# Kernel optimization log

Hardware: AMD Instinct MI355X
Metric: run time of the kernel (lower is better)

## Reference

```python
import jax, jax.numpy as jnp
import numpy as np

EPS = 1e-5
SLOPE = 0.2


def _conv(x, w, b, stride, pad):
    y = jax.lax.conv_general_dilated(
        x, w, (stride, stride), ((pad, pad), (pad, pad)),
        dimension_numbers=('NCHW', 'OIHW', 'NCHW'))
    return y + b[None, :, None, None]


def _inorm(x):
    m = x.mean(axis=(2, 3), keepdims=True)
    v = x.var(axis=(2, 3), keepdims=True)
    return (x - m) * jax.lax.rsqrt(v + EPS)


def _down(x, w, b, norm):
    y = _conv(x, w, b, 2, 1)
    if norm:
        y = _inorm(y)
    return jax.nn.leaky_relu(y, SLOPE)


def _self_attn(x, wq, bq, wk, bk, wv, bv, gamma):
    B, C, H, W = x.shape
    N = H * W
    q = _conv(x, wq, bq, 1, 0).reshape(B, -1, N)   # (B, C/8, N)
    k = _conv(x, wk, bk, 1, 0).reshape(B, -1, N)
    v = _conv(x, wv, bv, 1, 0).reshape(B, C, N)
    attn = jax.nn.softmax(jnp.einsum('bcn,bcm->bnm', q, k), axis=-1)  # (B,N,N)
    out = jnp.einsum('bcm,bnm->bcn', v, attn).reshape(B, C, H, W)
    return gamma * out + x


def _branch(p, img):
    (w0, b0, w1, b1, w2, b2, wq, bq, wk, bk, wv, bv, gamma, wh, bh) = p
    x = _down(img, w0, b0, norm=False)
    x = _down(x, w1, b1, norm=True)
    x = _self_attn(x, wq, bq, wk, bk, wv, bv, gamma)
    x = _down(x, w2, b2, norm=True)
    return _conv(x, wh, bh, 1, 1)  # head: Conv2d(nf*4, 1, 4, padding=1)


def setup_inputs() -> dict:
    key = jax.random.key(0)
    ks = jax.random.split(key, 20)
    S, B, H = 4, 16, 128
    s = 0.05  # weight scale for numerical stability of softmax energies
    d = {
        'img': jax.random.normal(ks[0], (B, 1, H, H), jnp.float32),
        'stage_idx': jax.random.randint(ks[1], (B,), 0, S, jnp.int32),
        'w0': jax.random.normal(ks[2], (S, 64, 1, 4, 4)) * s,
        'b0': jax.random.normal(ks[3], (S, 64)) * s,
        'w1': jax.random.normal(ks[4], (S, 128, 64, 4, 4)) * s,
        'b1': jax.random.normal(ks[5], (S, 128)) * s,
        'w2': jax.random.normal(ks[6], (S, 256, 128, 4, 4)) * s,
        'b2': jax.random.normal(ks[7], (S, 256)) * s,
        'wq': jax.random.normal(ks[8], (S, 16, 128, 1, 1)) * s,
        'bq': jax.random.normal(ks[9], (S, 16)) * s,
        'wk': jax.random.normal(ks[10], (S, 16, 128, 1, 1)) * s,
        'bk': jax.random.normal(ks[11], (S, 16)) * s,
        'wv': jax.random.normal(ks[12], (S, 128, 128, 1, 1)) * s,
        'bv': jax.random.normal(ks[13], (S, 128)) * s,
        'gamma': jax.random.normal(ks[14], (S,)) * s,
        'wh': jax.random.normal(ks[15], (S, 1, 256, 4, 4)) * s,
        'bh': jax.random.normal(ks[16], (S, 1)) * s,
    }
    return d


def reference(img, stage_idx, w0, b0, w1, b1, w2, b2, wq, bq, wk, bk, wv, bv, gamma, wh, bh):
    params = (w0, b0, w1, b1, w2, b2, wq, bq, wk, bk, wv, bv, gamma, wh, bh)
    # compute every branch for every sample (as the original), stacked over stage axis
    all_preds = jax.vmap(_branch, in_axes=(0, None))(params, img)  # (S, B, 1, h, w)
    B = img.shape[0]
    return all_preds[stage_idx, jnp.arange(B)]  # (B, 1, h, w)
```

## Files before the change

kernel.cpp:

```cpp
#include <hip/hip_runtime.h>

#define LRELU(x) ((x) > 0.0f ? (x) : 0.2f * (x))
#define SB __builtin_amdgcn_sched_barrier(0)

typedef short bf16x8 __attribute__((ext_vector_type(8)));
typedef short bf16x4 __attribute__((ext_vector_type(4)));
typedef float f32x4 __attribute__((ext_vector_type(4)));

__device__ __forceinline__ short f2bf(float f) {
  union { float f; unsigned u; } x{f};
  return (short)((x.u + 0x7FFF + ((x.u >> 16) & 1)) >> 16);
}

__global__ __launch_bounds__(256) void k_repack_all(
    const float* __restrict__ w1, unsigned short* __restrict__ wr1,
    const float* __restrict__ w2, unsigned short* __restrict__ wr2,
    const float* __restrict__ bh, const int* __restrict__ sidx,
    float* __restrict__ out, unsigned short* __restrict__ x0t,
    unsigned short* __restrict__ ybf, const float* __restrict__ img,
    const float* __restrict__ w0, const float* __restrict__ b0) {
  __shared__ float Ish[4 * 34];
  if (blockIdx.x >= 2837) {
    const int t = threadIdx.x;
    const int q = blockIdx.x - 2837;
    const int b = q >> 8, py = q & 255;
    const int oh = py >> 2, owb = (py & 3) << 4;
    const int s = sidx[b];
    const float* ip = img + (size_t)b * 16384;
    if (t < 136) {
      int r = t / 34, c = t % 34;
      int ih = 2 * oh - 1 + r, iw = 2 * owb - 1 + c;
      Ish[t] = ((unsigned)ih < 128u && (unsigned)iw < 128u) ? ip[ih * 128 + iw] : 0.f;
    }
    const int co = t & 63, ps = t >> 6;
    float wreg[16];
    const float* wp = w0 + (s * 64 + co) * 16;
#pragma unroll
    for (int i = 0; i < 16; i++) wreg[i] = wp[i];
    float bb = b0[s * 64 + co];
    __syncthreads();
    unsigned short* op = x0t + ((size_t)b * 4356 + (oh + 1) * 66 + (owb + 1)) * 64 + co;
#pragma unroll
    for (int j = 0; j < 4; j++) {
      int pl = ps * 4 + j;
      float acc = bb;
#pragma unroll
      for (int kh = 0; kh < 4; kh++)
#pragma unroll
        for (int kw = 0; kw < 4; kw++)
          acc += wreg[kh * 4 + kw] * Ish[kh * 34 + pl * 2 + kw];
      acc = LRELU(acc);
      op[pl * 64] = (unsigned short)f2bf(acc);
    }
    return;
  }
  int idx = blockIdx.x * 256 + threadIdx.x;
  if (idx < 131072) {
    float4 v = *(const float4*)(w1 + (size_t)idx * 4);
    int base = idx * 4;
    int tap0 = base & 15;
    int rest = base >> 4;
    int ci = rest & 63, sco = rest >> 6;
    unsigned short* d = wr1 + (size_t)sco * 1024 + ci;
    d[(tap0 + 0) * 64] = (unsigned short)f2bf(v.x);
    d[(tap0 + 1) * 64] = (unsigned short)f2bf(v.y);
    d[(tap0 + 2) * 64] = (unsigned short)f2bf(v.z);
    d[(tap0 + 3) * 64] = (unsigned short)f2bf(v.w);
    return;
  } else if (idx < 655360) {
    int i = idx - 131072;
    float4 v = *(const float4*)(w2 + (size_t)i * 4);
    int base = i * 4;
    int tap0 = base & 15;
    int rest = base >> 4;
    int ci = rest & 127, sco = rest >> 7;
    unsigned short* d = wr2 + (size_t)sco * 2048 + ci;
    d[(tap0 + 0) * 128] = (unsigned short)f2bf(v.x);
    d[(tap0 + 1) * 128] = (unsigned short)f2bf(v.y);
    d[(tap0 + 2) * 128] = (unsigned short)f2bf(v.z);
    d[(tap0 + 3) * 128] = (unsigned short)f2bf(v.w);
    return;
  } else if (idx < 658960) {
    int i = idx - 655360;
    if (i < 3600) out[i] = bh[sidx[i / 225]];
    return;
  } else if (idx < 692240) {
    int i = idx - 658960;
    int b = i / 2080, r = i % 2080;
    int pix = r >> 3, sub = r & 7;
    int row, col;
    if (pix < 66) { row = 0; col = pix; }
    else if (pix < 132) { row = 65; col = pix - 66; }
    else { int qq = pix - 132; row = 1 + (qq >> 1); col = (qq & 1) * 65; }
    bf16x8 z = {0, 0, 0, 0, 0, 0, 0, 0};
    *(bf16x8*)(x0t + ((size_t)b * 4356 + row * 66 + col) * 64 + sub * 8) = z;
    return;
  } else {
    int i = idx - 692240;
    if (i >= 33792) return;
    int b = i / 2112, r = i % 2112;
    int pix = r >> 4, sub = r & 15;
    int row, col;
    if (pix < 34) { row = 0; col = pix; }
    else if (pix < 68) { row = 33; col = pix - 34; }
    else { int qq = pix - 68; row = 1 + (qq >> 1); col = (qq & 1) * 33; }
    bf16x8 z = {0, 0, 0, 0, 0, 0, 0, 0};
    *(bf16x8*)(ybf + ((size_t)b * 1156 + row * 34 + col) * 128 + sub * 8) = z;
    return;
  }
}

__global__ __launch_bounds__(256, 2) void k_conv1n(
    const unsigned short* __restrict__ x0t, const unsigned short* __restrict__ wr,
    const int* __restrict__ sidx, float* __restrict__ x1) {
  __shared__ __align__(16) unsigned short Xs[26624];
  const int t = threadIdx.x;
  const int b = blockIdx.x;
  const int y = blockIdx.y;
  const int ne = y & 15;
  const int cog = y >> 4;
  const int s = sidx[b];
  const int lane = t & 63, wv = t >> 6;
  const int quad = lane >> 4, l16 = lane & 15;

  const unsigned short* gb = x0t + ((size_t)b * 4356 + 4 * ne * 66) * 64;
  {
    float4 v[13];
#pragma unroll
    for (int i = 0; i < 13; i++) v[i] = *(const float4*)(gb + (i * 256 + t) * 8);
#pragma unroll
    for (int i = 0; i < 13; i++) {
      int ba = (i * 256 + t) * 16;
      int sw = ba ^ (((ba >> 9) & 7) << 4);
      *(float4*)((char*)Xs + sw) = v[i];
    }
  }
  __syncthreads();

  const int co0w = cog * 64 + wv * 16;
  const unsigned short* ap = wr + ((size_t)(s * 128 + co0w + l16)) * 1024 + quad * 8;
  f32x4 acc[4];
#pragma unroll
  for (int nt = 0; nt < 4; nt++) acc[nt] = (f32x4){0.f, 0.f, 0.f, 0.f};

#pragma unroll
  for (int kc = 0; kc < 32; kc++) {
    const int tap = kc >> 1;
    const int cio = (kc & 1) * 32 + quad * 8;
    const int kh = tap >> 2, kw = tap & 3;
    bf16x8 af = *(const bf16x8*)(ap + kc * 32);
#pragma unroll
    for (int nt = 0; nt < 4; nt++) {
      int lr = 2 * (nt >> 1) + kh;
      int col = 2 * ((nt & 1) * 16 + l16) + kw;
      int ba = ((lr * 66 + col) * 64 + cio) * 2;
      int sw = ba ^ (((ba >> 9) & 7) << 4);
      bf16x8 bv = *(const bf16x8*)((const char*)Xs + sw);
      acc[nt] = __builtin_amdgcn_mfma_f32_16x16x32_bf16(af, bv, acc[nt], 0, 0, 0);
    }
  }

#pragma unroll
  for (int nt = 0; nt < 4; nt++) {
    int p = ne * 64 + (nt >> 1) * 32 + (nt & 1) * 16 + l16;
#pragma unroll
    for (int r = 0; r < 4; r++)
      x1[((size_t)b * 128 + co0w + quad * 4 + r) * 1024 + p] = acc[nt][r];
  }
}

template <int NPIX>
__global__ __launch_bounds__(256) void k_inorm(float* __restrict__ x) {
  constexpr int E = NPIX / 256;
  float* p = x + (size_t)blockIdx.x * NPIX;
  const int t = threadIdx.x;
  float v[E];
  float sum = 0.f, sq = 0.f;
#pragma unroll
  for (int i = 0; i < E; i++) {
    v[i] = p[i * 256 + t];
    sum += v[i];
    sq += v[i] * v[i];
  }
#pragma unroll
  for (int o = 32; o > 0; o >>= 1) {
    sum += __shfl_down(sum, o, 64);
    sq += __shfl_down(sq, o, 64);
  }
  __shared__ float red[8];
  int wid = t >> 6;
  if ((t & 63) == 0) {
    red[wid] = sum;
    red[4 + wid] = sq;
  }
  __syncthreads();
  float S = red[0] + red[1] + red[2] + red[3];
  float SQ = red[4] + red[5] + red[6] + red[7];
  float m = S * (1.0f / NPIX);
  float var = SQ * (1.0f / NPIX) - m * m;
  float inv = rsqrtf(var + 1e-5f);
#pragma unroll
  for (int i = 0; i < E; i++) p[i * 256 + t] = LRELU((v[i] - m) * inv);
}

__global__ __launch_bounds__(256) void k_proj_qkv(
    const float* __restrict__ xin, const float* __restrict__ wq,
    const float* __restrict__ bq, const float* __restrict__ wk,
    const float* __restrict__ bk, const float* __restrict__ wv,
    const float* __restrict__ bv, const int* __restrict__ sidx,
    float* __restrict__ q, float* __restrict__ kout, unsigned short* __restrict__ vpk) {
  __shared__ float xsh[32 * 256];
  __shared__ float wsh[16 * 32];
  const int t = threadIdx.x;
  const int b = blockIdx.x;
  const int y = blockIdx.y;
  const int s = sidx[b];
  const int cg = t >> 6, ng = t & 63;
  const float* w;
  const float* bias;
  int co0, nn0, CO;
  if (y < 8) {
    w = (y < 4) ? wq : wk;
    bias = (y < 4) ? bq : bk;
    co0 = 0;
    nn0 = (y & 3) * 256;
    CO = 16;
  } else {
    w = wv;
    bias = bv;
    co0 = ((y - 8) >> 2) * 16;
    nn0 = ((y - 8) & 3) * 256;
    CO = 128;
  }
  const float* xb = xin + (size_t)b * 128 * 1024;
  float4 acc4[4];
#pragma unroll
  for (int c = 0; c < 4; c++) {
    float bb = bias[s * CO + co0 + cg * 4 + c];
    acc4[c] = make_float4(bb, bb, bb, bb);
  }
  for (int cc = 0; cc < 4; cc++) {
#pragma unroll
    for (int k = 0; k < 8; k++) {
      int id = t + (k << 8);
      int ci = id >> 6, nf = id & 63;
      ((float4*)xsh)[id] = ((const float4*)(xb + (cc * 32 + ci) * 1024 + nn0))[nf];
    }
    if (t < 128)
      ((float4*)wsh)[t] =
          ((const float4*)(w + ((size_t)(s * CO + co0 + (t >> 3))) * 128 + cc * 32))[t & 7];
    __syncthreads();
#pragma unroll
    for (int ci4 = 0; ci4 < 8; ci4++) {
      float4 wvv[4], xv[4];
#pragma unroll
      for (int c = 0; c < 4; c++) wvv[c] = ((const float4*)wsh)[(cg * 4 + c) * 8 + ci4];
#pragma unroll
      for (int i = 0; i < 4; i++) xv[i] = ((const float4*)xsh)[(ci4 * 4 + i) * 64 + ng];
#pragma unroll
      for (int c = 0; c < 4; c++)
#pragma unroll
        for (int i = 0; i < 4; i++) {
          float wvc = i == 0 ? wvv[c].x : i == 1 ? wvv[c].y : i == 2 ? wvv[c].z : wvv[c].w;
          acc4[c].x += wvc * xv[i].x;
          acc4[c].y += wvc * xv[i].y;
          acc4[c].z += wvc * xv[i].z;
          acc4[c].w += wvc * xv[i].w;
        }
    }
    __syncthreads();
  }
  if (y < 8) {
    float* out = (y < 4) ? q : kout;
#pragma unroll
    for (int c = 0; c < 4; c++)
      ((float4*)(out + ((size_t)b * 16 + cg * 4 + c) * 1024 + nn0))[ng] = acc4[c];
  } else {
    int n = nn0 + ng * 4;
#pragma unroll
    for (int c = 0; c < 4; c++) {
      int co = co0 + cg * 4 + c;
      bf16x4 u;
      u[0] = f2bf(acc4[c].x);
      u[1] = f2bf(acc4[c].y);
      u[2] = f2bf(acc4[c].z);
      u[3] = f2bf(acc4[c].w);
      *(bf16x4*)(vpk + (((size_t)b * 32 + (n >> 5)) * 128 + co) * 32 + (n & 31)) = u;
    }
  }
}

__global__ __launch_bounds__(256, 2) void k_attn(
    const float* __restrict__ q, const float* __restrict__ k,
    const unsigned short* __restrict__ vpk, const float* __restrict__ x1,
    const float* __restrict__ gamma, const int* __restrict__ sidx,
    unsigned short* __restrict__ ybf) {
  __shared__ __align__(16) short Psh[16 * 1032];
  __shared__ float qsh[256];
  __shared__ float redm[64], reds[64];
  const int t = threadIdx.x;
  const int b = blockIdx.x >> 6;
  const int n0 = (blockIdx.x & 63) << 4;
  const int lane = t & 63, wv = t >> 6;
  const int quad = lane >> 4, l16 = lane & 15;
  const float* qb = q + (size_t)b * 16 * 1024;
  const float* kb = k + (size_t)b * 16 * 1024;
  const float* xb = x1 + (size_t)b * 128 * 1024;

  qsh[t] = qb[((t >> 4) << 10) + n0 + (t & 15)];
  __syncthreads();

  float acc[4][16];
#pragma unroll
  for (int j = 0; j < 4; j++)
#pragma unroll
    for (int nl = 0; nl < 16; nl++) acc[j][nl] = 0.0f;

  float4 KA[4], KB[4];
#define LDK(BUF, G)                                                       \
  _Pragma("unroll") for (int c4 = 0; c4 < 4; c4++)                        \
      BUF[c4] = *(const float4*)(kb + ((((G) * 4 + c4)) << 10) + 4 * t);  \
  SB;
#define MMK(BUF, G)                                                                         \
  _Pragma("unroll") for (int c4 = 0; c4 < 4; c4++) {                                        \
    const float* qr = qsh + ((G) * 4 + c4) * 16;                                            \
    _Pragma("unroll") for (int j = 0; j < 4; j++) {                                         \
      float kk = j == 0 ? BUF[c4].x : j == 1 ? BUF[c4].y : j == 2 ? BUF[c4].z : BUF[c4].w;  \
      _Pragma("unroll") for (int nl = 0; nl < 16; nl++) acc[j][nl] += kk * qr[nl];          \
    }                                                                                       \
  }                                                                                         \
  SB;

  LDK(KA, 0)
  LDK(KB, 1)
  MMK(KA, 0) LDK(KA, 2)
  MMK(KB, 1) LDK(KB, 3)
  MMK(KA, 2)
  MMK(KB, 3)
#undef LDK
#undef MMK

  float lmax[16];
#pragma unroll
  for (int nl = 0; nl < 16; nl++)
    lmax[nl] = fmaxf(fmaxf(acc[0][nl], acc[1][nl]), fmaxf(acc[2][nl], acc[3][nl]));
#pragma unroll
  for (int o = 32; o > 0; o >>= 1)
#pragma unroll
    for (int nl = 0; nl < 16; nl++) lmax[nl] = fmaxf(lmax[nl], __shfl_xor(lmax[nl], o, 64));
  if (lane == 0)
#pragma unroll
    for (int nl = 0; nl < 16; nl++) redm[wv * 16 + nl] = lmax[nl];
  __syncthreads();
#pragma unroll
  for (int nl = 0; nl < 16; nl++)
    lmax[nl] = fmaxf(fmaxf(redm[nl], redm[16 + nl]), fmaxf(redm[32 + nl], redm[48 + nl]));
  float lsum[16];
#pragma unroll
  for (int nl = 0; nl < 16; nl++) lsum[nl] = 0.0f;
#pragma unroll
  for (int j = 0; j < 4; j++)
#pragma unroll
    for (int nl = 0; nl < 16; nl++) {
      float e = __expf(acc[j][nl] - lmax[nl]);
      acc[j][nl] = e;
      lsum[nl] += e;
    }
#pragma unroll
  for (int o = 32; o > 0; o >>= 1)
#pragma unroll
    for (int nl = 0; nl < 16; nl++) lsum[nl] += __shfl_xor(lsum[nl], o, 64);
  if (lane == 0)
#pragma unroll
    for (int nl = 0; nl < 16; nl++) reds[wv * 16 + nl] = lsum[nl];
#pragma unroll
  for (int nl = 0; nl < 16; nl++) {
    bf16x4 pv;
    pv[0] = f2bf(acc[0][nl]);
    pv[1] = f2bf(acc[1][nl]);
    pv[2] = f2bf(acc[2][nl]);
    pv[3] = f2bf(acc[3][nl]);
    *(bf16x4*)&Psh[nl * 1032 + 4 * t] = pv;
  }
  __syncthreads();

  const unsigned short* vp =
      vpk + ((size_t)b * 32 * 128 + (size_t)(wv * 32 + l16)) * 32 + quad * 8;
  const short* prow = Psh + l16 * 1032 + quad * 8;
  f32x4 dacc[2];
  dacc[0] = (f32x4){0.f, 0.f, 0.f, 0.f};
  dacc[1] = (f32x4){0.f, 0.f, 0.f, 0.f};

  bf16x8 VA0[4], VA1[4], PAr[4];
  bf16x8 VB0[4], VB1[4], PBr[4];
#define LDV(V0, V1, PR, G)                                \
  _Pragma("unroll") for (int m4 = 0; m4 < 4; m4++) {      \
    int mt = (G) * 4 + m4;                                \
    V0[m4] = *(const bf16x8*)(vp + mt * 4096);            \
    V1[m4] = *(const bf16x8*)(vp + 512 + mt * 4096);      \
    PR[m4] = *(const bf16x8*)(prow + mt * 32);            \
  }                                                       \
  SB;
#define MMV(V0, V1, PR)                                                                      \
  _Pragma("unroll") for (int m4 = 0; m4 < 4; m4++) {                                         \
    dacc[0] = __builtin_amdgcn_mfma_f32_16x16x32_bf16(V0[m4], PR[m4], dacc[0], 0, 0, 0);     \
    dacc[1] = __builtin_amdgcn_mfma_f32_16x16x32_bf16(V1[m4], PR[m4], dacc[1], 0, 0, 0);     \
  }                                                                                          \
  SB;

  LDV(VA0, VA1, PAr, 0)
  LDV(VB0, VB1, PBr, 1)
  MMV(VA0, VA1, PAr) LDV(VA0, VA1, PAr, 2)
  MMV(VB0, VB1, PBr) LDV(VB0, VB1, PBr, 3)
  MMV(VA0, VA1, PAr) LDV(VA0, VA1, PAr, 4)
  MMV(VB0, VB1, PBr) LDV(VB0, VB1, PBr, 5)
  MMV(VA0, VA1, PAr) LDV(VA0, VA1, PAr, 6)
  MMV(VB0, VB1, PBr) LDV(VB0, VB1, PBr, 7)
  MMV(VA0, VA1, PAr)
  MMV(VB0, VB1, PBr)
#undef LDV
#undef MMV
  __syncthreads();

  float* Osh = (float*)Psh;
  short* Osh2 = Psh + 4352;
#pragma unroll
  for (int i = 0; i < 2; i++) {
    int cob = wv * 32 + i * 16 + quad * 4;
#pragma unroll
    for (int r = 0; r < 4; r++) Osh[(cob + r) * 17 + l16] = dacc[i][r];
  }
  __syncthreads();
  float g = gamma[sidx[b]];
  {
    int co = t >> 1, j0 = (t & 1) * 8;
    const float* xr = xb + (co << 10) + n0 + j0;
    float4 xv0 = *(const float4*)xr;
    float4 xv1 = *(const float4*)(xr + 4);
    float xs[8] = {xv0.x, xv0.y, xv0.z, xv0.w, xv1.x, xv1.y, xv1.z, xv1.w};
#pragma unroll
    for (int j = 0; j < 8; j++) {
      int nl = j0 + j;
      float rs = 1.0f / (reds[nl] + reds[16 + nl] + reds[32 + nl] + reds[48 + nl]);
      Osh2[nl * 136 + co] = f2bf(g * Osh[co * 17 + nl] * rs + xs[j]);
    }
  }
  __syncthreads();
  {
    int nl = t >> 4, cg = t & 15;
    bf16x8 u = *(const bf16x8*)&Osh2[nl * 136 + cg * 8];
    int p = n0 + nl;
    int ih = p >> 5, iw = p & 31;
    *(bf16x8*)(ybf + ((size_t)b * 1156 + (ih + 1) * 34 + (iw + 1)) * 128 + cg * 8) = u;
  }
}

__global__ __launch_bounds__(256, 2) void k_conv2n(
    const unsigned short* __restrict__ ybf, const unsigned short* __restrict__ wr,
    const int* __restrict__ sidx, float* __restrict__ x2) {
  __shared__ __align__(16) unsigned short Xs[26624];
  const int t = threadIdx.x;
  const int b = blockIdx.x;
  const int y = blockIdx.y;
  const int ne = y & 7;
  const int cog = y >> 3;
  const int s = sidx[b];
  const int lane = t & 63, wv = t >> 6;
  const int quad = lane >> 4, l16 = lane & 15;

  const unsigned short* gb = ybf + ((size_t)b * 1156 + 4 * ne * 34) * 128;
  {
    float4 v[13];
#pragma unroll
    for (int i = 0; i < 13; i++) v[i] = *(const float4*)(gb + (i * 256 + t) * 8);
#pragma unroll
    for (int i = 0; i < 13; i++) {
      int ba = (i * 256 + t) * 16;
      int sw = ba ^ (((ba >> 9) & 7) << 4);
      *(float4*)((char*)Xs + sw) = v[i];
    }
  }
  __syncthreads();

  const int co0w = cog * 64 + wv * 16;
  const unsigned short* ap = wr + ((size_t)(s * 256 + co0w + l16)) * 2048 + quad * 8;
  f32x4 acc[2];
  acc[0] = (f32x4){0.f, 0.f, 0.f, 0.f};
  acc[1] = (f32x4){0.f, 0.f, 0.f, 0.f};

#pragma unroll
  for (int kc = 0; kc < 64; kc++) {
    const int tap = kc >> 2;
    const int cio = (kc & 3) * 32 + quad * 8;
    const int kh = tap >> 2, kw = tap & 3;
    bf16x8 af = *(const bf16x8*)(ap + kc * 32);
#pragma unroll
    for (int nt = 0; nt < 2; nt++) {
      int lr = 2 * nt + kh;
      int col = 2 * l16 + kw;
      int ba = ((lr * 34 + col) * 128 + cio) * 2;
      int sw = ba ^ (((ba >> 9) & 7) << 4);
      bf16x8 bv = *(const bf16x8*)((const char*)Xs + sw);
      acc[nt] = __builtin_amdgcn_mfma_f32_16x16x32_bf16(af, bv, acc[nt], 0, 0, 0);
    }
  }

#pragma unroll
  for (int nt = 0; nt < 2; nt++) {
    int p = ne * 32 + nt * 16 + l16;
#pragma unroll
    for (int r = 0; r < 4; r++)
      x2[((size_t)b * 256 + co0w + quad * 4 + r) * 256 + p] = acc[nt][r];
  }
}

__global__ __launch_bounds__(256) void k_head_part(
    const float* __restrict__ x2, const float* __restrict__ wh,
    const int* __restrict__ sidx, float* __restrict__ out) {
  __shared__ float Xs[32 * 256];
  __shared__ float Wsh[512];
  __shared__ float sm[32], si[32];
  const int t = threadIdx.x;
  const int b = blockIdx.x, cc = blockIdx.y;
  const int s = sidx[b];
  const float* xp = x2 + ((size_t)b * 256 + cc * 32) * 256;
#pragma unroll
  for (int i = 0; i < 32; i++) Xs[i * 256 + t] = xp[i * 256 + t];
#pragma unroll
  for (int i = 0; i < 2; i++) {
    int idx = i * 256 + t;
    Wsh[idx] = wh[s * 4096 + cc * 512 + idx];
  }
  __syncthreads();
  {
    int r = t >> 3, c0 = (t & 7) * 32;
    float sv = 0.f, sq = 0.f;
#pragma unroll
    for (int j = 0; j < 32; j++) {
      float v = Xs[r * 256 + c0 + j];
      sv += v;
      sq += v * v;
    }
#pragma unroll
    for (int o = 1; o < 8; o <<= 1) {
      sv += __shfl_xor(sv, o, 64);
      sq += __shfl_xor(sq, o, 64);
    }
    if ((t & 7) == 0) {
      float m = sv * (1.0f / 256.0f);
      float var = sq * (1.0f / 256.0f) - m * m;
      sm[r] = m;
      si[r] = rsqrtf(var + 1e-5f);
    }
  }
  __syncthreads();
#pragma unroll
  for (int i = 0; i < 32; i++) {
    float v = (Xs[i * 256 + t] - sm[i]) * si[i];
    Xs[i * 256 + t] = LRELU(v);
  }
  __syncthreads();
  if (t < 225) {
    int oh = t / 15, ow = t % 15;
    float acc = 0.0f;
    for (int ci = 0; ci < 32; ci++) {
      const float* xr = Xs + ci * 256;
      const float* wr = Wsh + ci * 16;
#pragma unroll
      for (int kh = 0; kh < 4; kh++) {
        int ih = oh - 1 + kh;
        if ((unsigned)ih >= 16u) continue;
#pragma unroll
        for (int kw = 0; kw < 4; kw++) {
          int iw = ow - 1 + kw;
          if ((unsigned)iw >= 16u) continue;
          acc += wr[kh * 4 + kw] * xr[(ih << 4) + iw];
        }
      }
    }
    atomicAdd(out + b * 225 + t, acc);
  }
}

extern "C" void kernel_launch(void* const* d_in, const int* in_sizes, int n_in,
                              void* d_out, int out_size, void* d_ws, size_t ws_size,
                              hipStream_t stream) {
  const float* img = (const float*)d_in[0];
  const int* sidx = (const int*)d_in[1];
  const float* w0 = (const float*)d_in[2];
  const float* b0 = (const float*)d_in[3];
  const float* w1 = (const float*)d_in[4];
  const float* w2 = (const float*)d_in[6];
  const float* wq = (const float*)d_in[8];
  const float* bq = (const float*)d_in[9];
  const float* wk = (const float*)d_in[10];
  const float* bk = (const float*)d_in[11];
  const float* wv = (const float*)d_in[12];
  const float* bv = (const float*)d_in[13];
  const float* gamma = (const float*)d_in[14];
  const float* wh = (const float*)d_in[15];
  const float* bh = (const float*)d_in[16];
  float* out = (float*)d_out;

  float* ws = (float*)d_ws;
  unsigned short* x0t = (unsigned short*)(ws);
  float* x1 = ws + 2359296;
  float* q = ws + 4456448;
  float* k = ws + 4718592;
  unsigned short* vpk = (unsigned short*)(ws + 4980736);
  unsigned short* ybf = (unsigned short*)(ws + 6029312);
  float* x2 = ws + 7340032;
  unsigned short* wr1 = (unsigned short*)(ws + 8912896);
  unsigned short* wr2 = (unsigned short*)(ws + 9175040);

  const int B = 16;

  k_repack_all<<<6933, 256, 0, stream>>>(w1, wr1, w2, wr2, bh, sidx, out, x0t, ybf,
                                         img, w0, b0);
  k_conv1n<<<dim3(B, 32), 256, 0, stream>>>(x0t, wr1, sidx, x1);
  k_inorm<1024><<<B * 128, 256, 0, stream>>>(x1);
  k_proj_qkv<<<dim3(B, 40), 256, 0, stream>>>(x1, wq, bq, wk, bk, wv, bv, sidx, q, k, vpk);
  k_attn<<<B * 64, 256, 0, stream>>>(q, k, vpk, x1, gamma, sidx, ybf);
  k_conv2n<<<dim3(B, 32), 256, 0, stream>>>(ybf, wr2, sidx, x2);
  k_head_part<<<dim3(B, 8), 256, 0, stream>>>(x2, wh, sidx, out);
}
```

Measured before the change: 201.0 us.

## Fuse instance-norm stats into conv1 epilogue and apply normalization in consumers

Removes the standalone instance-norm kernel. Conv1 now reduces per-channel sum and sum-of-squares with shuffles and atomically accumulates them into a stat buffer, which the repack kernel zeroes. The QKV projection and attention kernels then apply normalization and LeakyReLU on the fly when reading raw x1. This saves a full read/write pass over x1 and one launch, at the cost of atomics and duplicated normalization math in two consumers.

```diff
diff --git a/kernel.cpp b/kernel.cpp
--- a/kernel.cpp
+++ b/kernel.cpp
@@ -18,11 +18,12 @@
     const float* __restrict__ bh, const int* __restrict__ sidx,
     float* __restrict__ out, unsigned short* __restrict__ x0t,
     unsigned short* __restrict__ ybf, const float* __restrict__ img,
-    const float* __restrict__ w0, const float* __restrict__ b0) {
+    const float* __restrict__ w0, const float* __restrict__ b0,
+    float* __restrict__ stat) {
   __shared__ float Ish[4 * 34];
-  if (blockIdx.x >= 2837) {
+  if (blockIdx.x >= 2853) {
     const int t = threadIdx.x;
-    const int q = blockIdx.x - 2837;
+    const int q = blockIdx.x - 2853;
     const int b = q >> 8, py = q & 255;
     const int oh = py >> 2, owb = (py & 3) << 4;
     const int s = sidx[b];
@@ -95,7 +96,7 @@
     bf16x8 z = {0, 0, 0, 0, 0, 0, 0, 0};
     *(bf16x8*)(x0t + ((size_t)b * 4356 + row * 66 + col) * 64 + sub * 8) = z;
     return;
-  } else {
+  } else if (idx < 726032) {
     int i = idx - 692240;
     if (i >= 33792) return;
     int b = i / 2112, r = i % 2112;
@@ -107,12 +108,17 @@
     bf16x8 z = {0, 0, 0, 0, 0, 0, 0, 0};
     *(bf16x8*)(ybf + ((size_t)b * 1156 + row * 34 + col) * 128 + sub * 8) = z;
     return;
+  } else {
+    int i = idx - 726032;
+    if (i < 4096) stat[i] = 0.f;
+    return;
   }
 }
 
 __global__ __launch_bounds__(256, 2) void k_conv1n(
     const unsigned short* __restrict__ x0t, const unsigned short* __restrict__ wr,
-    const int* __restrict__ sidx, float* __restrict__ x1) {
+    const int* __restrict__ sidx, float* __restrict__ x1,
+    float* __restrict__ stat) {
   __shared__ __align__(16) unsigned short Xs[26624];
   const int t = threadIdx.x;
   const int b = blockIdx.x;
@@ -161,46 +167,29 @@
   }
 
 #pragma unroll
+  for (int r = 0; r < 4; r++) {
+    float sv = acc[0][r] + acc[1][r] + acc[2][r] + acc[3][r];
+    float sq = acc[0][r] * acc[0][r] + acc[1][r] * acc[1][r] +
+               acc[2][r] * acc[2][r] + acc[3][r] * acc[3][r];
+#pragma unroll
+    for (int o = 1; o < 16; o <<= 1) {
+      sv += __shfl_xor(sv, o, 64);
+      sq += __shfl_xor(sq, o, 64);
+    }
+    if (l16 == 0) {
+      int co = co0w + quad * 4 + r;
+      atomicAdd(&stat[(b * 128 + co) * 2 + 0], sv);
+      atomicAdd(&stat[(b * 128 + co) * 2 + 1], sq);
+    }
+  }
+
+#pragma unroll
   for (int nt = 0; nt < 4; nt++) {
     int p = ne * 64 + (nt >> 1) * 32 + (nt & 1) * 16 + l16;
 #pragma unroll
     for (int r = 0; r < 4; r++)
       x1[((size_t)b * 128 + co0w + quad * 4 + r) * 1024 + p] = acc[nt][r];
   }
-}
-
-template <int NPIX>
-__global__ __launch_bounds__(256) void k_inorm(float* __restrict__ x) {
-  constexpr int E = NPIX / 256;
-  float* p = x + (size_t)blockIdx.x * NPIX;
-  const int t = threadIdx.x;
-  float v[E];
-  float sum = 0.f, sq = 0.f;
-#pragma unroll
-  for (int i = 0; i < E; i++) {
-    v[i] = p[i * 256 + t];
-    sum += v[i];
-    sq += v[i] * v[i];
-  }
-#pragma unroll
-  for (int o = 32; o > 0; o >>= 1) {
-    sum += __shfl_down(sum, o, 64);
-    sq += __shfl_down(sq, o, 64);
-  }
-  __shared__ float red[8];
-  int wid = t >> 6;
-  if ((t & 63) == 0) {
-    red[wid] = sum;
-    red[4 + wid] = sq;
-  }
-  __syncthreads();
-  float S = red[0] + red[1] + red[2] + red[3];
-  float SQ = red[4] + red[5] + red[6] + red[7];
-  float m = S * (1.0f / NPIX);
-  float var = SQ * (1.0f / NPIX) - m * m;
-  float inv = rsqrtf(var + 1e-5f);
-#pragma unroll
-  for (int i = 0; i < E; i++) p[i * 256 + t] = LRELU((v[i] - m) * inv);
 }
 
 __global__ __launch_bounds__(256) void k_proj_qkv(
@@ -208,9 +197,11 @@
     const float* __restrict__ bq, const float* __restrict__ wk,
     const float* __restrict__ bk, const float* __restrict__ wv,
     const float* __restrict__ bv, const int* __restrict__ sidx,
+    const float* __restrict__ stat,
     float* __restrict__ q, float* __restrict__ kout, unsigned short* __restrict__ vpk) {
   __shared__ float xsh[32 * 256];
   __shared__ float wsh[16 * 32];
+  __shared__ float msh[128], ish[128];
   const int t = threadIdx.x;
   const int b = blockIdx.x;
   const int y = blockIdx.y;
@@ -232,6 +223,14 @@
     nn0 = ((y - 8) & 3) * 256;
     CO = 128;
   }
+  if (t < 128) {
+    float sv = stat[(b * 128 + t) * 2 + 0];
+    float sq = stat[(b * 128 + t) * 2 + 1];
+    float m = sv * (1.0f / 1024.0f);
+    float var = sq * (1.0f / 1024.0f) - m * m;
+    msh[t] = m;
+    ish[t] = rsqrtf(var + 1e-5f);
+  }
   const float* xb = xin + (size_t)b * 128 * 1024;
   float4 acc4[4];
 #pragma unroll
@@ -239,12 +238,19 @@
     float bb = bias[s * CO + co0 + cg * 4 + c];
     acc4[c] = make_float4(bb, bb, bb, bb);
   }
+  __syncthreads();
   for (int cc = 0; cc < 4; cc++) {
 #pragma unroll
     for (int k = 0; k < 8; k++) {
       int id = t + (k << 8);
       int ci = id >> 6, nf = id & 63;
-      ((float4*)xsh)[id] = ((const float4*)(xb + (cc * 32 + ci) * 1024 + nn0))[nf];
+      float4 v = ((const float4*)(xb + (cc * 32 + ci) * 1024 + nn0))[nf];
+      float m = msh[cc * 32 + ci], iv = ish[cc * 32 + ci];
+      v.x = (v.x - m) * iv; v.x = LRELU(v.x);
+      v.y = (v.y - m) * iv; v.y = LRELU(v.y);
+      v.z = (v.z - m) * iv; v.z = LRELU(v.z);
+      v.w = (v.w - m) * iv; v.w = LRELU(v.w);
+      ((float4*)xsh)[id] = v;
     }
     if (t < 128)
       ((float4*)wsh)[t] =
@@ -294,7 +300,7 @@
     const float* __restrict__ q, const float* __restrict__ k,
     const unsigned short* __restrict__ vpk, const float* __restrict__ x1,
     const float* __restrict__ gamma, const int* __restrict__ sidx,
-    unsigned short* __restrict__ ybf) {
+    const float* __restrict__ stat, unsigned short* __restrict__ ybf) {
   __shared__ __align__(16) short Psh[16 * 1032];
   __shared__ float qsh[256];
   __shared__ float redm[64], reds[64];
@@ -434,10 +440,19 @@
   float g = gamma[sidx[b]];
   {
     int co = t >> 1, j0 = (t & 1) * 8;
+    float sv = stat[(b * 128 + co) * 2 + 0];
+    float sq = stat[(b * 128 + co) * 2 + 1];
+    float mm = sv * (1.0f / 1024.0f);
+    float iv = rsqrtf(sq * (1.0f / 1024.0f) - mm * mm + 1e-5f);
     const float* xr = xb + (co << 10) + n0 + j0;
     float4 xv0 = *(const float4*)xr;
     float4 xv1 = *(const float4*)(xr + 4);
     float xs[8] = {xv0.x, xv0.y, xv0.z, xv0.w, xv1.x, xv1.y, xv1.z, xv1.w};
+#pragma unroll
+    for (int j = 0; j < 8; j++) {
+      float nv = (xs[j] - mm) * iv;
+      xs[j] = LRELU(nv);
+    }
 #pragma unroll
     for (int j = 0; j < 8; j++) {
       int nl = j0 + j;
@@ -610,17 +625,18 @@
   unsigned short* vpk = (unsigned short*)(ws + 4980736);
   unsigned short* ybf = (unsigned short*)(ws + 6029312);
   float* x2 = ws + 7340032;
+  float* stat = ws + 8650752;
   unsigned short* wr1 = (unsigned short*)(ws + 8912896);
   unsigned short* wr2 = (unsigned short*)(ws + 9175040);
 
   const int B = 16;
 
-  k_repack_all<<<6933, 256, 0, stream>>>(w1, wr1, w2, wr2, bh, sidx, out, x0t, ybf,
-                                         img, w0, b0);
-  k_conv1n<<<dim3(B, 32), 256, 0, stream>>>(x0t, wr1, sidx, x1);
-  k_inorm<1024><<<B * 128, 256, 0, stream>>>(x1);
-  k_proj_qkv<<<dim3(B, 40), 256, 0, stream>>>(x1, wq, bq, wk, bk, wv, bv, sidx, q, k, vpk);
-  k_attn<<<B * 64, 256, 0, stream>>>(q, k, vpk, x1, gamma, sidx, ybf);
+  k_repack_all<<<6949, 256, 0, stream>>>(w1, wr1, w2, wr2, bh, sidx, out, x0t, ybf,
+                                         img, w0, b0, stat);
+  k_conv1n<<<dim3(B, 32), 256, 0, stream>>>(x0t, wr1, sidx, x1, stat);
+  k_proj_qkv<<<dim3(B, 40), 256, 0, stream>>>(x1, wq, bq, wk, bk, wv, bv, sidx, stat,
+                                              q, k, vpk);
+  k_attn<<<B * 64, 256, 0, stream>>>(q, k, vpk, x1, gamma, sidx, stat, ybf);
   k_conv2n<<<dim3(B, 32), 256, 0, stream>>>(ybf, wr2, sidx, x2);
   k_head_part<<<dim3(B, 8), 256, 0, stream>>>(x2, wh, sidx, out);
 }
```

New measurement: 197.6 us. No clear change (-1.7%).
